# Kernel optimization log

Measured on AMD Instinct MI355X. Metric: run time of the kernel, lower is better.

The kernel has to match this reference:

```python
import jax, jax.numpy as jnp
import numpy as np

B, C, H, W = 128, 128, 32, 32
EPS = 1e-5


def _proj(x, w, b):
    # 1x1 conv: w [C_out, C_in], b [C_out]
    return jnp.einsum('oi,bihw->bohw', w, x) + b[None, :, None, None]


def _conv(x, w, pad):
    # x [B,Cin,H,W], w [Cout,Cin,k,k]
    return jax.lax.conv_general_dilated(
        x, w, window_strides=(1, 1), padding=[(pad, pad), (pad, pad)],
        dimension_numbers=('NCHW', 'OIHW', 'NCHW'))


def _ln(x, g, b):
    # LayerNorm over [C,H,W] per batch element
    mu = jnp.mean(x, axis=(1, 2, 3), keepdims=True)
    var = jnp.var(x, axis=(1, 2, 3), keepdims=True)
    return (x - mu) * jax.lax.rsqrt(var + EPS) * g[None] + b[None]


def _attn(q, k, v):
    # per (b,c) spatial matmul: [H,W]@[W,W] -> softmax -> @[W,W] -> softmax
    a = jax.nn.softmax(jnp.einsum('bchw,bcwk->bchk', q, k), axis=-1)
    return jax.nn.softmax(jnp.einsum('bchw,bcwk->bchk', a, v), axis=-1)


def setup_inputs() -> dict:
    key = jax.random.key(0)
    ks = iter(jax.random.split(key, 32))
    d = {}
    d['st'] = jax.random.normal(next(ks), (B, C, H, W), jnp.float32)
    d['phy'] = jax.random.normal(next(ks), (B, C, H, W), jnp.float32)
    s = 1.0 / np.sqrt(C)
    for nm in ['q_st', 'k_st', 'v_st', 'q_phy', 'k_phy', 'v_phy']:
        d['w' + nm] = jax.random.normal(next(ks), (C, C), jnp.float32) * s
        d['b' + nm] = jnp.zeros((C,), jnp.float32)
    for kk, nm in [(3, '3'), (5, '5'), (7, '7'), (1, '1')]:
        fan = 4 * C * kk * kk
        d['w' + nm] = jax.random.normal(next(ks), (C, 4 * C, kk, kk), jnp.float32) / np.sqrt(fan)
        d['g' + nm] = jnp.ones((C, H, W), jnp.float32)
        d['be' + nm] = jnp.zeros((C, H, W), jnp.float32)
    d['b1'] = jnp.zeros((C,), jnp.float32)
    return d


def reference(st, phy,
              wq_st, bq_st, wk_st, bk_st, wv_st, bv_st,
              wq_phy, bq_phy, wk_phy, bk_phy, wv_phy, bv_phy,
              w3, g3, be3, w5, g5, be5, w7, g7, be7,
              w1, b1, g1, be1):
    q_phy = _proj(phy, wq_phy, bq_phy)
    k_phy = _proj(phy, wk_phy, bk_phy)
    v_phy = _proj(phy, wv_phy, bv_phy)
    out_phy = _attn(q_phy, k_phy, v_phy) + phy

    q_st = _proj(st, wq_st, bq_st)
    k_st = _proj(st, wk_st, bk_st)
    v_st = _proj(st, wv_st, bv_st)
    out_st = _attn(q_st, k_st, v_st) + st

    out_st_phy = _attn(q_phy, k_st, v_st)
    out_phy_st = _attn(q_st, k_phy, v_phy)

    concat = jnp.concatenate([out_st, out_phy, out_st_phy, out_phy_st], axis=1)

    x1 = _ln(_conv(concat, w3, 1), g3, be3)
    x2 = _ln(_conv(concat, w5, 2), g5, be5)
    x3 = _ln(_conv(concat, w7, 3), g7, be7)
    out_mti = jax.nn.sigmoid((x1 + x2 + x3) / 3.0)
    out_att = _ln(_conv(concat, w1, 0) + b1[None, :, None, None], g1, be1)
    return out_mti + out_att
```

## Files before the change

### kernel.cpp

```cpp
#include <hip/hip_runtime.h>
#include <hip/hip_bf16.h>

typedef __hip_bfloat16 bf16;
typedef unsigned char u8;
typedef unsigned long long u64;
typedef __attribute__((ext_vector_type(8))) short short8;
typedef __attribute__((ext_vector_type(8))) int i32x8;
typedef __attribute__((ext_vector_type(16))) float f32x16;
#define DI __device__ __forceinline__

union BF8 { int4 v; short8 s; bf16 h[8]; };
union BF4 { u64 u; bf16 h[4]; };
union U32B { int4 v[2]; i32x8 w; };


DI u8 f32_fp8(float v) {
  return (u8)(__builtin_amdgcn_cvt_pk_fp8_f32(v, 0.f, 0, false) & 0xff);
}

__global__ __launch_bounds__(256) void prep_w_kernel(
    const float* __restrict__ w3, const float* __restrict__ w5,
    const float* __restrict__ w7, const float* __restrict__ w1,
    const float* __restrict__ wq_st, const float* __restrict__ wk_st,
    const float* __restrict__ wv_st, const float* __restrict__ wq_phy,
    const float* __restrict__ wk_phy, const float* __restrict__ wv_phy,
    u8* __restrict__ wf3, u8* __restrict__ wf5,
    u8* __restrict__ wf7, bf16* __restrict__ wb1, bf16* __restrict__ wp)
{
  const int N3 = 9 * 65536, N5 = 25 * 65536, N7 = 49 * 65536, N1 = 65536;
  const int NP = 6 * 16384;
  const int total = N3 + N5 + N7 + N1 + NP;
  for (int i = blockIdx.x * 256 + threadIdx.x; i < total; i += gridDim.x * 256) {
    if (i < N3 + N5 + N7) {
      const float* w; int k; int taps;
      u8* dst;
      if (i < N3)           { w = w3; k = i;            taps = 9;  dst = wf3; }
      else if (i < N3 + N5) { w = w5; k = i - N3;       taps = 25; dst = wf5; }
      else                  { w = w7; k = i - N3 - N5;  taps = 49; dst = wf7; }
      int tap = k >> 16, rem = k & 65535;
      int cc2 = rem >> 13, r2 = rem & 8191;
      int g = r2 >> 12, r3 = r2 & 4095;
      int oc = r3 >> 5, o = r3 & 31;
      int ic = (cc2 * 2 + g) * 32 + ((o >> 3) & 1) * 16 + ((o >> 4) & 1) * 8 + (o & 7);
      dst[k] = f32_fp8(w[(size_t)(oc * 512 + ic) * taps + tap] * 256.0f);
    } else if (i < N3 + N5 + N7 + N1) {
      int k = i - N3 - N5 - N7;
      int icg = k >> 10, oc = (k >> 3) & 127, j = k & 7;
      wb1[k] = __float2bfloat16(w1[(size_t)oc * 512 + icg * 8 + j]);
    } else {
      int k = i - N3 - N5 - N7 - N1;
      int m = k >> 14, r = k & 16383;
      float v;
      switch (m) {
        case 0: v = wq_st[r]; break;
        case 1: v = wk_st[r]; break;
        case 2: v = wv_st[r]; break;
        case 3: v = wq_phy[r]; break;
        case 4: v = wk_phy[r]; break;
        default: v = wv_phy[r]; break;
      }
      wp[k] = __float2bfloat16(v);
    }
  }
}

__global__ __launch_bounds__(256) void xpose_in_kernel(
    const float* __restrict__ st, const float* __restrict__ phy,
    bf16* __restrict__ Xt)
{
  __shared__ __align__(16) short Tb[64 * 72];
  const int x = blockIdx.x, b = blockIdx.y;
  const int t = x >> 5, rem = x & 31;
  const int ict = rem >> 4, post = rem & 15;
  const int ic0 = ict * 64, pos0 = post * 64;
  const int tid = threadIdx.x;
  const int rowi = tid >> 2, sub = tid & 3;
  const float* X = t ? phy : st;

  const float* src = X + ((size_t)b * 128 + ic0 + rowi) * 1024 + pos0 + sub * 16;
  #pragma unroll
  for (int q = 0; q < 4; ++q) {
    float4 v = *(const float4*)(src + q * 4);
    BF4 pk;
    pk.h[0] = __float2bfloat16(v.x); pk.h[1] = __float2bfloat16(v.y);
    pk.h[2] = __float2bfloat16(v.z); pk.h[3] = __float2bfloat16(v.w);
    *(u64*)&Tb[rowi * 72 + sub * 16 + q * 4] = pk.u;
  }
  __syncthreads();
  short tmp[16];
  #pragma unroll
  for (int j = 0; j < 16; ++j) tmp[j] = Tb[(sub * 16 + j) * 72 + rowi];
  bf16* dst = Xt + (((size_t)t * 128 + b) * 1024 + pos0 + rowi) * 128 + ic0 + sub * 16;
  *(int4*)dst       = ((int4*)tmp)[0];
  *(int4*)(dst + 8) = ((int4*)tmp)[1];
}

__global__ __launch_bounds__(256) void proj_mfma(
    const bf16* __restrict__ Xt, const bf16* __restrict__ wproj,
    const float* __restrict__ b0, const float* __restrict__ b1,
    const float* __restrict__ b2, const float* __restrict__ b3,
    const float* __restrict__ b4, const float* __restrict__ b5,
    bf16* __restrict__ pc, int cb)
{
  const int pt = blockIdx.x, b = blockIdx.y;
  const int tid = threadIdx.x, wave = tid >> 6, lane = tid & 63;
  const int col = lane & 31, kg = lane >> 5;
  const int pos = pt * 128 + wave * 32 + col;

  f32x16 acc[6];
  #pragma unroll
  for (int m = 0; m < 6; ++m)
    #pragma unroll
    for (int e = 0; e < 16; ++e) acc[m][e] = 0.f;

  const bf16* xst = Xt + ((size_t)b * 1024 + pos) * 128 + kg * 8;
  const bf16* xph = xst + (size_t)128 * 1024 * 128;
  const bf16* wl = wproj + (size_t)(cb + col) * 128 + kg * 8;

  #pragma unroll
  for (int kst = 0; kst < 8; ++kst) {
    short8 bst = *(const short8*)&xst[kst * 16];
    short8 bph = *(const short8*)&xph[kst * 16];
    #pragma unroll
    for (int m = 0; m < 6; ++m) {
      BF8 a; a.v = *(const int4*)&wl[(size_t)m * 16384 + kst * 16];
      acc[m] = __builtin_amdgcn_mfma_f32_32x32x16_bf16(a.s, m < 3 ? bst : bph, acc[m], 0, 0, 0);
    }
  }
  const float* biases[6] = { b0, b1, b2, b3, b4, b5 };
  #pragma unroll
  for (int m = 0; m < 6; ++m) {
    #pragma unroll
    for (int r = 0; r < 16; ++r) {
      const int ocl = (r & 3) + 8 * (r >> 2) + 4 * kg;
      float v = acc[m][r] + biases[m][cb + ocl];
      pc[(((size_t)m * 128 + b) * 32 + ocl) * 1024 + pos] = __float2bfloat16(v);
    }
  }
}

DI void softmax_rows(float p[16])
{
  #pragma unroll
  for (int r = 0; r < 16; ++r) {
    float m = p[r];
    m = fmaxf(m, __shfl_xor(m, 1));
    m = fmaxf(m, __shfl_xor(m, 2));
    m = fmaxf(m, __shfl_xor(m, 4));
    m = fmaxf(m, __shfl_xor(m, 8));
    m = fmaxf(m, __shfl_xor(m, 16));
    float e = __expf(p[r] - m);
    float s = e;
    s += __shfl_xor(s, 1); s += __shfl_xor(s, 2); s += __shfl_xor(s, 4);
    s += __shfl_xor(s, 8); s += __shfl_xor(s, 16);
    p[r] = __fdividef(e, s);
  }
}

template<bool U8OUT>
DI void attn_one_mfma(const BF8& qa0, const BF8& qa1,
                      const bf16* __restrict__ KT, const bf16* __restrict__ VT,
                      bf16* __restrict__ P,
                      const float* __restrict__ resid, void* outp, int lane)
{
  const int col = lane & 31, kg = lane >> 5;
  f32x16 acc;
  #pragma unroll
  for (int e = 0; e < 16; ++e) acc[e] = 0.f;
  BF8 kb0, kb1;
  kb0.v = *(const int4*)&KT[col * 40 + kg * 8];
  kb1.v = *(const int4*)&KT[col * 40 + 16 + kg * 8];
  acc = __builtin_amdgcn_mfma_f32_32x32x16_bf16(qa0.s, kb0.s, acc, 0, 0, 0);
  acc = __builtin_amdgcn_mfma_f32_32x32x16_bf16(qa1.s, kb1.s, acc, 0, 0, 0);
  float p[16];
  #pragma unroll
  for (int r = 0; r < 16; ++r) p[r] = acc[r];
  softmax_rows(p);
  __syncthreads();
  #pragma unroll
  for (int r = 0; r < 16; ++r) {
    int row = (r & 3) + 8 * (r >> 2) + 4 * kg;
    P[row * 40 + col] = __float2bfloat16(p[r]);
  }
  __syncthreads();
  BF8 pa0, pa1, vb0, vb1;
  pa0.v = *(const int4*)&P[col * 40 + kg * 8];
  pa1.v = *(const int4*)&P[col * 40 + 16 + kg * 8];
  vb0.v = *(const int4*)&VT[col * 40 + kg * 8];
  vb1.v = *(const int4*)&VT[col * 40 + 16 + kg * 8];
  #pragma unroll
  for (int e = 0; e < 16; ++e) acc[e] = 0.f;
  acc = __builtin_amdgcn_mfma_f32_32x32x16_bf16(pa0.s, vb0.s, acc, 0, 0, 0);
  acc = __builtin_amdgcn_mfma_f32_32x32x16_bf16(pa1.s, vb1.s, acc, 0, 0, 0);
  #pragma unroll
  for (int r = 0; r < 16; ++r) p[r] = acc[r];
  softmax_rows(p);
  if constexpr (!U8OUT) {
    bf16* op = (bf16*)outp;
    #pragma unroll
    for (int r = 0; r < 16; ++r) {
      int row = (r & 3) + 8 * (r >> 2) + 4 * kg;
      int off = row * 32 + col;
      op[off] = __float2bfloat16(p[r] + resid[off]);
    }
  } else {
    u8* op = (u8*)outp;
    #pragma unroll
    for (int r = 0; r < 16; ++r) {
      int row = (r & 3) + 8 * (r >> 2) + 4 * kg;
      op[row * 32 + col] = (u8)fminf(p[r] * 256.f + 0.5f, 255.f);
    }
  }
}

__global__ __launch_bounds__(64) void attn_mfma_kernel(
    const bf16* __restrict__ pc,
    const float* __restrict__ st, const float* __restrict__ phy,
    bf16* __restrict__ cA, u8* __restrict__ cB, int cb)
{
  __shared__ __align__(16) bf16 KTst[32 * 40], VTst[32 * 40];
  __shared__ __align__(16) bf16 KTph[32 * 40], VTph[32 * 40];
  __shared__ __align__(16) bf16 P[32 * 40];
  const int cl = blockIdx.x, b = blockIdx.y;
  const int c = cb + cl;
  const int lane = threadIdx.x;
  const size_t mstride = (size_t)128 * 32 * 1024;
  const bf16* p0 = pc + ((size_t)b * 32 + cl) * 1024;
  const size_t bc = ((size_t)b * 128 + c) * 1024;

  {
    const int w = lane >> 1, k0 = (lane & 1) * 16;
    const int off = w * 32 + k0;
    bf16* dsts[4] = { KTst, VTst, KTph, VTph };
    const int ms[4] = { 1, 2, 4, 5 };
    #pragma unroll
    for (int t = 0; t < 4; ++t) {
      BF8 r0, r1;
      r0.v = *(const int4*)&p0[(size_t)ms[t] * mstride + off];
      r1.v = *(const int4*)&p0[(size_t)ms[t] * mstride + off + 8];
      #pragma unroll
      for (int j = 0; j < 8; ++j) {
        dsts[t][(k0 + j) * 40 + w]     = r0.h[j];
        dsts[t][(k0 + 8 + j) * 40 + w] = r1.h[j];
      }
    }
  }
  const int col = lane & 31, kg = lane >> 5;
  BF8 qst0, qst1, qph0, qph1;
  qst0.v = *(const int4*)&p0[col * 32 + kg * 8];
  qst1.v = *(const int4*)&p0[col * 32 + 16 + kg * 8];
  qph0.v = *(const int4*)&p0[3 * mstride + col * 32 + kg * 8];
  qph1.v = *(const int4*)&p0[3 * mstride + col * 32 + 16 + kg * 8];
  __syncthreads();

  bf16* aA = cA + (size_t)b * 256 * 1024 + (size_t)c * 1024;
  u8*   aB = cB + (size_t)b * 256 * 1024 + (size_t)c * 1024;
  attn_one_mfma<false>(qst0, qst1, KTst, VTst, P, st + bc,  aA,          lane);
  attn_one_mfma<false>(qph0, qph1, KTph, VTph, P, phy + bc, aA + 131072, lane);
  attn_one_mfma<true >(qph0, qph1, KTst, VTst, P, nullptr,  aB,          lane);
  attn_one_mfma<true >(qst0, qst1, KTph, VTph, P, nullptr,  aB + 131072, lane);
}

__global__ __launch_bounds__(256) void transpose_kernel(
    const bf16* __restrict__ cA, const u8* __restrict__ cB,
    bf16* __restrict__ cAT, u8* __restrict__ cBT)
{
  __shared__ __align__(16) short Tb[64 * 72];
  __shared__ __align__(16) u8 T8[64 * 80];
  const int x = blockIdx.x, b = blockIdx.y;
  const int cht = x >> 4, post = x & 15;
  const int pos0 = post * 64;
  const int tid = threadIdx.x;
  const int rowi = tid >> 2, sub = tid & 3;

  if (cht < 4) {
    const int ch0 = cht * 64;
    const bf16* src = cA + ((size_t)b * 256 + ch0 + rowi) * 1024 + pos0 + sub * 16;
    *(int4*)&Tb[rowi * 72 + sub * 16]     = *(const int4*)src;
    *(int4*)&Tb[rowi * 72 + sub * 16 + 8] = *(const int4*)(src + 8);
    __syncthreads();
    short tmp[16];
    #pragma unroll
    for (int j = 0; j < 16; ++j) tmp[j] = Tb[(sub * 16 + j) * 72 + rowi];
    bf16* dst = cAT + ((size_t)b * 1024 + pos0 + rowi) * 256 + ch0 + sub * 16;
    *(int4*)dst       = ((int4*)tmp)[0];
    *(int4*)(dst + 8) = ((int4*)tmp)[1];
  } else {
    const int ch0 = (cht - 4) * 64;
    const u8* src = cB + ((size_t)b * 256 + ch0 + rowi) * 1024 + pos0 + sub * 16;
    *(int4*)&T8[rowi * 80 + sub * 16] = *(const int4*)src;
    __syncthreads();
    u8 tmp[16];
    #pragma unroll
    for (int j = 0; j < 16; ++j) tmp[j] = T8[(sub * 16 + j) * 80 + rowi];
    u8* dst = cBT + ((size_t)b * 1024 + pos0 + rowi) * 256 + ch0 + sub * 16;
    *(int4*)dst = *(int4*)tmp;
  }
}

__global__ __launch_bounds__(256) void to_fp8_kernel(
    const bf16* __restrict__ cAT, const u8* __restrict__ cBT,
    u8* __restrict__ cAT8)
{
  const int idx = blockIdx.x * 256 + threadIdx.x;
  const int g = idx & 31;
  const size_t bp = (size_t)(idx >> 5);
  const int c0 = g * 16;
  float v[16];
  if (c0 < 256) {
    BF8 lo, hi;
    lo.v = *(const int4*)&cAT[bp * 256 + c0];
    hi.v = *(const int4*)&cAT[bp * 256 + c0 + 8];
    #pragma unroll
    for (int j = 0; j < 8; ++j) {
      v[j]     = __bfloat162float(lo.h[j]) * 16.0f;
      v[8 + j] = __bfloat162float(hi.h[j]) * 16.0f;
    }
  } else {
    u64 raw0 = *(const u64*)&cBT[bp * 256 + (c0 - 256)];
    u64 raw1 = *(const u64*)&cBT[bp * 256 + (c0 - 256) + 8];
    #pragma unroll
    for (int j = 0; j < 8; ++j) {
      v[j]     = (float)((raw0 >> (8 * j)) & 255u) * 0.0625f;
      v[8 + j] = (float)((raw1 >> (8 * j)) & 255u) * 0.0625f;
    }
  }
  unsigned lo0 = (__builtin_amdgcn_cvt_pk_fp8_f32(v[0], v[1], 0, false) & 0xffff)
               | ((__builtin_amdgcn_cvt_pk_fp8_f32(v[2], v[3], 0, false) & 0xffff) << 16);
  unsigned hi0 = (__builtin_amdgcn_cvt_pk_fp8_f32(v[4], v[5], 0, false) & 0xffff)
               | ((__builtin_amdgcn_cvt_pk_fp8_f32(v[6], v[7], 0, false) & 0xffff) << 16);
  unsigned lo1 = (__builtin_amdgcn_cvt_pk_fp8_f32(v[8], v[9], 0, false) & 0xffff)
               | ((__builtin_amdgcn_cvt_pk_fp8_f32(v[10], v[11], 0, false) & 0xffff) << 16);
  unsigned hi1 = (__builtin_amdgcn_cvt_pk_fp8_f32(v[12], v[13], 0, false) & 0xffff)
               | ((__builtin_amdgcn_cvt_pk_fp8_f32(v[14], v[15], 0, false) & 0xffff) << 16);
  u64 run0 = (u64)lo0 | ((u64)hi0 << 32);
  u64 run1 = (u64)lo1 | ((u64)hi1 << 32);
  const int sp = (c0 >> 4) & 1;
  u8* d = cAT8 + bp * 512 + (c0 & ~31);
  *(u64*)(d + 8 * sp)      = run0;
  *(u64*)(d + 16 + 8 * sp) = run1;
}

template<int PCX, int NIT, int H0>
DI void stage_tile(const bf16* cAT, const u8* cBT, short* Xs,
                   int b, int r0, int ic0, int tid)
{
  for (int e = tid; e < NIT; e += 256) {
    int i = e / (PCX * 4);
    int rem = e - i * (PCX * 4);
    int cx = rem >> 2, part = rem & 3;
    int ir = r0 - H0 + i, c = cx - H0;
    int4 val = make_int4(0, 0, 0, 0);
    if ((unsigned)ir < 32u && (unsigned)c < 32u) {
      size_t pbase = ((size_t)b * 1024 + ir * 32 + c) * 256;
      if (ic0 < 256) {
        val = *(const int4*)&cAT[pbase + ic0 + part * 8];
      } else {
        u64 u = *(const u64*)&cBT[pbase + (ic0 - 256) + part * 8];
        BF8 t;
        #pragma unroll
        for (int j = 0; j < 8; ++j)
          t.h[j] = __float2bfloat16((float)((u >> (8 * j)) & 255u) * 0.00390625f);
        val = t.v;
      }
    }
    *(int4*)&Xs[(i * PCX + cx) * 40 + part * 8] = val;
  }
}

template<int KS>
__global__ __launch_bounds__(256, 2) void conv_mfma(
    const bf16* __restrict__ cAT, const u8* __restrict__ cBT,
    const bf16* __restrict__ wt, const float* __restrict__ bias,
    bf16* __restrict__ xout, float* __restrict__ partials)
{
  constexpr int H0 = KS / 2;
  constexpr int PCX = 32 + 2 * H0;
  constexpr int ROWS = 16 + 2 * H0;
  constexpr int NIT = ROWS * PCX * 4;
  __shared__ __align__(16) short Xs[ROWS * PCX * 40];
  __shared__ float rs[256], rq[256];
  const int h = blockIdx.x;
  const int logical = (h & 7) * 64 + (h >> 3);
  const int b = logical >> 2, tix = logical & 3;
  const int ot = tix >> 1, rt = tix & 1;
  const int oc0 = ot * 64, r0 = rt * 16;
  const int tid = threadIdx.x;
  const int wv = tid >> 6, lane = tid & 63;
  const int col = lane & 31, kg = lane >> 5;

  f32x16 acc[2][4];
  #pragma unroll
  for (int i = 0; i < 2; ++i)
    #pragma unroll
    for (int j = 0; j < 4; ++j)
      #pragma unroll
      for (int e = 0; e < 16; ++e) acc[i][j][e] = 0.f;

  for (int cc = 0; cc < 16; ++cc) {
    const int ic0 = cc * 32;
    stage_tile<PCX, NIT, H0>(cAT, cBT, Xs, b, r0, ic0, tid);
    __syncthreads();

    #pragma unroll 1
    for (int ky = 0; ky < KS; ++ky) {
      #pragma unroll
      for (int kx = 0; kx < KS; ++kx) {
        const int tap = ky * KS + kx;
        BF8 a[2][2];
        #pragma unroll
        for (int ob = 0; ob < 2; ++ob)
          #pragma unroll
          for (int kt = 0; kt < 2; ++kt) {
            int icg = cc * 4 + kt * 2 + kg;
            a[ob][kt].v = *(const int4*)&wt[(((size_t)tap * 64 + icg) * 128 + oc0 + ob * 32 + col) * 8];
          }
        #pragma unroll
        for (int rr = 0; rr < 4; ++rr) {
          int entry = ((wv * 4 + rr + ky) * PCX + col + kx) * 40;
          #pragma unroll
          for (int kt = 0; kt < 2; ++kt) {
            short8 bf = *(const short8*)&Xs[entry + (kt * 2 + kg) * 8];
            acc[0][rr] = __builtin_amdgcn_mfma_f32_32x32x16_bf16(a[0][kt].s, bf, acc[0][rr], 0, 0, 0);
            acc[1][rr] = __builtin_amdgcn_mfma_f32_32x32x16_bf16(a[1][kt].s, bf, acc[1][rr], 0, 0, 0);
          }
        }
      }
    }
    __syncthreads();
  }

  float lsum = 0.f, lsq = 0.f;
  #pragma unroll
  for (int ob = 0; ob < 2; ++ob)
    #pragma unroll
    for (int rr = 0; rr < 4; ++rr) {
      const int row = r0 + wv * 4 + rr;
      #pragma unroll
      for (int r = 0; r < 16; ++r) {
        const int oc = oc0 + ob * 32 + (r & 3) + 8 * (r >> 2) + 4 * kg;
        float v = acc[ob][rr][r];
        if (bias) v += bias[oc];
        xout[((size_t)b * 128 + oc) * 1024 + row * 32 + col] = __float2bfloat16(v);
        lsum += v; lsq += v * v;
      }
    }
  rs[tid] = lsum; rq[tid] = lsq;
  __syncthreads();
  for (int s = 128; s > 0; s >>= 1) {
    if (tid < s) { rs[tid] += rs[tid + s]; rq[tid] += rq[tid + s]; }
    __syncthreads();
  }
  if (tid == 0) {
    partials[((size_t)b * 4 + tix) * 2]     = rs[0];
    partials[((size_t)b * 4 + tix) * 2 + 1] = rq[0];
  }
}

template<int KS>
__global__ __launch_bounds__(256, 2) void conv_mx(
    const u8* __restrict__ cAT8, const u8* __restrict__ wf,
    bf16* __restrict__ xout, float* __restrict__ partials)
{
  constexpr int H0 = KS / 2;
  constexpr int PCX = 32 + 2 * H0;
  constexpr int ROWS = 16 + 2 * H0;
  constexpr int NIT = ROWS * PCX * 4;
  __shared__ __align__(16) u8 Xs[ROWS * PCX * 80];
  __shared__ float rs[256], rq[256];
  const int h = blockIdx.x;
  const int logical = (h & 7) * 64 + (h >> 3);
  const int b = logical >> 2, tix = logical & 3;
  const int ot = tix >> 1, rt = tix & 1;
  const int oc0 = ot * 64, r0 = rt * 16;
  const int tid = threadIdx.x;
  const int wv = tid >> 6, lane = tid & 63;
  const int col = lane & 31, g = lane >> 5;

  f32x16 acc[2][4];
  #pragma unroll
  for (int i = 0; i < 2; ++i)
    #pragma unroll
    for (int j = 0; j < 4; ++j)
      #pragma unroll
      for (int e = 0; e < 16; ++e) acc[i][j][e] = 0.f;

  for (int cc2 = 0; cc2 < 8; ++cc2) {
    for (int e = tid; e < NIT; e += 256) {
      int entry = e >> 2, hf = e & 3;
      int i = entry / PCX, cx = entry - i * PCX;
      int ir = r0 - H0 + i, c = cx - H0;
      int4 val = make_int4(0, 0, 0, 0);
      if ((unsigned)ir < 32u && (unsigned)c < 32u)
        val = *(const int4*)&cAT8[((size_t)b * 1024 + ir * 32 + c) * 512 + cc2 * 64 + hf * 16];
      *(int4*)&Xs[entry * 80 + hf * 16] = val;
    }
    __syncthreads();

    #pragma unroll 1
    for (int ky = 0; ky < KS; ++ky) {
      #pragma unroll
      for (int kx = 0; kx < KS; ++kx) {
        const int tap = ky * KS + kx;
        const size_t wbase = (((size_t)tap * 8 + cc2) * 2 + g) * 128;
        U32B a0, a1;
        a0.v[0] = *(const int4*)&wf[(wbase + oc0 + col) * 32];
        a0.v[1] = *(const int4*)&wf[(wbase + oc0 + col) * 32 + 16];
        a1.v[0] = *(const int4*)&wf[(wbase + oc0 + 32 + col) * 32];
        a1.v[1] = *(const int4*)&wf[(wbase + oc0 + 32 + col) * 32 + 16];
        #pragma unroll
        for (int rr = 0; rr < 4; ++rr) {
          const int ebase = ((wv * 4 + rr + ky) * PCX + col + kx) * 80 + g * 32;
          U32B bf;
          bf.v[0] = *(const int4*)&Xs[ebase];
          bf.v[1] = *(const int4*)&Xs[ebase + 16];
          acc[0][rr] = __builtin_amdgcn_mfma_scale_f32_32x32x64_f8f6f4(
              a0.w, bf.w, acc[0][rr], 0, 0, 0, 0x7f7f7f7f, 0, 0x7f7f7f7f);
          acc[1][rr] = __builtin_amdgcn_mfma_scale_f32_32x32x64_f8f6f4(
              a1.w, bf.w, acc[1][rr], 0, 0, 0, 0x7f7f7f7f, 0, 0x7f7f7f7f);
        }
      }
    }
    __syncthreads();
  }

  float lsum = 0.f, lsq = 0.f;
  #pragma unroll
  for (int ob = 0; ob < 2; ++ob)
    #pragma unroll
    for (int rr = 0; rr < 4; ++rr) {
      const int row = r0 + wv * 4 + rr;
      #pragma unroll
      for (int r = 0; r < 16; ++r) {
        const int oc = oc0 + ob * 32 + (r & 3) + 8 * (r >> 2) + 4 * g;
        float v = acc[ob][rr][r] * (1.0f / 4096.0f);
        xout[((size_t)b * 128 + oc) * 1024 + row * 32 + col] = __float2bfloat16(v);
        lsum += v; lsq += v * v;
      }
    }
  rs[tid] = lsum; rq[tid] = lsq;
  __syncthreads();
  for (int s = 128; s > 0; s >>= 1) {
    if (tid < s) { rs[tid] += rs[tid + s]; rq[tid] += rq[tid + s]; }
    __syncthreads();
  }
  if (tid == 0) {
    partials[((size_t)b * 4 + tix) * 2]     = rs[0];
    partials[((size_t)b * 4 + tix) * 2 + 1] = rq[0];
  }
}

__global__ __launch_bounds__(256) void final_kernel(
    const bf16* __restrict__ x3, const bf16* __restrict__ x5,
    const bf16* __restrict__ x7, const bf16* __restrict__ x1c,
    const float* __restrict__ p3, const float* __restrict__ p5,
    const float* __restrict__ p7, const float* __restrict__ p1,
    const float* __restrict__ g3, const float* __restrict__ be3,
    const float* __restrict__ g5, const float* __restrict__ be5,
    const float* __restrict__ g7, const float* __restrict__ be7,
    const float* __restrict__ g1, const float* __restrict__ be1,
    float* __restrict__ out)
{
  const int blk = blockIdx.x, b = blockIdx.y, tid = threadIdx.x;
  float s3 = 0, q3 = 0, s5 = 0, q5 = 0, s7 = 0, q7 = 0, s1 = 0, q1 = 0;
  #pragma unroll
  for (int i = 0; i < 4; ++i) {
    int o = (b * 4 + i) * 2;
    s3 += p3[o]; q3 += p3[o + 1];
    s5 += p5[o]; q5 += p5[o + 1];
    s7 += p7[o]; q7 += p7[o + 1];
    s1 += p1[o]; q1 += p1[o + 1];
  }
  const float inv = 1.0f / 131072.0f;
  float mu3 = s3 * inv, r3 = rsqrtf(fmaxf(q3 * inv - mu3 * mu3, 0.f) + 1e-5f);
  float mu5 = s5 * inv, r5 = rsqrtf(fmaxf(q5 * inv - mu5 * mu5, 0.f) + 1e-5f);
  float mu7 = s7 * inv, r7 = rsqrtf(fmaxf(q7 * inv - mu7 * mu7, 0.f) + 1e-5f);
  float mu1 = s1 * inv, r1 = rsqrtf(fmaxf(q1 * inv - mu1 * mu1, 0.f) + 1e-5f);
  const size_t bb = (size_t)b * 131072;
  for (int it = 0; it < 8; ++it) {
    int e0 = (it * 2048 + blk * 256 + tid) * 8;
    BF8 a3, a5, a7, a1;
    a3.v = *(const int4*)&x3[bb + e0];
    a5.v = *(const int4*)&x5[bb + e0];
    a7.v = *(const int4*)&x7[bb + e0];
    a1.v = *(const int4*)&x1c[bb + e0];
    float G3[8], B3[8], G5[8], B5[8], G7[8], B7[8], G1[8], B1[8];
    *(float4*)&G3[0] = *(const float4*)&g3[e0];  *(float4*)&G3[4] = *(const float4*)&g3[e0 + 4];
    *(float4*)&B3[0] = *(const float4*)&be3[e0]; *(float4*)&B3[4] = *(const float4*)&be3[e0 + 4];
    *(float4*)&G5[0] = *(const float4*)&g5[e0];  *(float4*)&G5[4] = *(const float4*)&g5[e0 + 4];
    *(float4*)&B5[0] = *(const float4*)&be5[e0]; *(float4*)&B5[4] = *(const float4*)&be5[e0 + 4];
    *(float4*)&G7[0] = *(const float4*)&g7[e0];  *(float4*)&G7[4] = *(const float4*)&g7[e0 + 4];
    *(float4*)&B7[0] = *(const float4*)&be7[e0]; *(float4*)&B7[4] = *(const float4*)&be7[e0 + 4];
    *(float4*)&G1[0] = *(const float4*)&g1[e0];  *(float4*)&G1[4] = *(const float4*)&g1[e0 + 4];
    *(float4*)&B1[0] = *(const float4*)&be1[e0]; *(float4*)&B1[4] = *(const float4*)&be1[e0 + 4];
    float res[8];
    #pragma unroll
    for (int j = 0; j < 8; ++j) {
      float v3 = (__bfloat162float(a3.h[j]) - mu3) * r3 * G3[j] + B3[j];
      float v5 = (__bfloat162float(a5.h[j]) - mu5) * r5 * G5[j] + B5[j];
      float v7 = (__bfloat162float(a7.h[j]) - mu7) * r7 * G7[j] + B7[j];
      float m = (v3 + v5 + v7) * (1.0f / 3.0f);
      float sg = 1.0f / (1.0f + __expf(-m));
      float v1 = (__bfloat162float(a1.h[j]) - mu1) * r1 * G1[j] + B1[j];
      res[j] = sg + v1;
    }
    *(float4*)&out[bb + e0]     = make_float4(res[0], res[1], res[2], res[3]);
    *(float4*)&out[bb + e0 + 4] = make_float4(res[4], res[5], res[6], res[7]);
  }
}

extern "C" void kernel_launch(void* const* d_in, const int* in_sizes, int n_in,
                              void* d_out, int out_size, void* d_ws, size_t ws_size,
                              hipStream_t stream)
{
  (void)in_sizes; (void)n_in; (void)out_size; (void)ws_size;
  const float* st     = (const float*)d_in[0];
  const float* phy    = (const float*)d_in[1];
  const float* wq_st  = (const float*)d_in[2];
  const float* bq_st  = (const float*)d_in[3];
  const float* wk_st  = (const float*)d_in[4];
  const float* bk_st  = (const float*)d_in[5];
  const float* wv_st  = (const float*)d_in[6];
  const float* bv_st  = (const float*)d_in[7];
  const float* wq_phy = (const float*)d_in[8];
  const float* bq_phy = (const float*)d_in[9];
  const float* wk_phy = (const float*)d_in[10];
  const float* bk_phy = (const float*)d_in[11];
  const float* wv_phy = (const float*)d_in[12];
  const float* bv_phy = (const float*)d_in[13];
  const float* w3  = (const float*)d_in[14];
  const float* g3  = (const float*)d_in[15];
  const float* be3 = (const float*)d_in[16];
  const float* w5  = (const float*)d_in[17];
  const float* g5  = (const float*)d_in[18];
  const float* be5 = (const float*)d_in[19];
  const float* w7  = (const float*)d_in[20];
  const float* g7  = (const float*)d_in[21];
  const float* be7 = (const float*)d_in[22];
  const float* w1  = (const float*)d_in[23];
  const float* g1  = (const float*)d_in[24];
  const float* be1 = (const float*)d_in[25];
  const float* b1  = (const float*)d_in[26];

  char* ws = (char*)d_ws;
  bf16* Xt        = (bf16*)ws;
  bf16* projchunk = (bf16*)(ws + 67108864ULL);
  bf16* cA        = (bf16*)(ws + 117440512ULL);
  u8*   cB        = (u8*)(ws + 184549376ULL);
  bf16* wproj     = (bf16*)(ws + 218103808ULL);
  bf16* cAT       = (bf16*)ws;
  u8*   cBT       = (u8*)(ws + 67108864ULL);
  u8*   cAT8      = (u8*)(ws + 117440512ULL);
  bf16* x1b       = (bf16*)(ws + 184549376ULL);
  bf16* x3b       = (bf16*)ws;
  bf16* x5b       = (bf16*)(ws + 33554432ULL);
  bf16* x7b       = (bf16*)(ws + 67108864ULL);
  float* parts    = (float*)(ws + 234881024ULL);
  u8*   wf3       = (u8*)(ws + 234913792ULL);
  u8*   wf5       = (u8*)(ws + 236093440ULL);
  u8*   wf7       = (u8*)(ws + 239370240ULL);
  bf16* wb1       = (bf16*)(ws + 245792768ULL);

  prep_w_kernel<<<dim3(2048), 256, 0, stream>>>(w3, w5, w7, w1,
      wq_st, wk_st, wv_st, wq_phy, wk_phy, wv_phy,
      wf3, wf5, wf7, wb1, wproj);
  xpose_in_kernel<<<dim3(64, 128), 256, 0, stream>>>(st, phy, Xt);

  for (int g = 0; g < 4; ++g) {
    proj_mfma<<<dim3(8, 128), 256, 0, stream>>>(Xt, wproj,
        bq_st, bk_st, bv_st, bq_phy, bk_phy, bv_phy, projchunk, g * 32);
    attn_mfma_kernel<<<dim3(32, 128), 64, 0, stream>>>(projchunk, st, phy,
        cA, cB, g * 32);
  }
  transpose_kernel<<<dim3(128, 128), 256, 0, stream>>>(cA, cB, cAT, cBT);
  to_fp8_kernel<<<dim3(16384), 256, 0, stream>>>(cAT, cBT, cAT8);

  conv_mfma<1><<<dim3(512), 256, 0, stream>>>(cAT, cBT, wb1, b1, x1b, parts + 6144);
  conv_mx<3><<<dim3(512), 256, 0, stream>>>(cAT8, wf3, x3b, parts);
  conv_mx<5><<<dim3(512), 256, 0, stream>>>(cAT8, wf5, x5b, parts + 2048);
  conv_mx<7><<<dim3(512), 256, 0, stream>>>(cAT8, wf7, x7b, parts + 4096);

  final_kernel<<<dim3(8, 128), 256, 0, stream>>>(x3b, x5b, x7b, x1b,
      parts, parts + 2048, parts + 4096, parts + 6144,
      g3, be3, g5, be5, g7, be7, g1, be1, (float*)d_out);
}
```

Baseline: 1.233 ms.

## Retile conv_mx blocks to all 128 output channels over 8 rows

Each block of the fp8 MFMA conv now covers all 128 output channels for an 8-row strip, where it used to cover 64 channels for a 16-row strip. Each wave loads its two input-row fragments from LDS once per tap and reuses them across four weight fragments. The smaller LDS halo tile allows three blocks per CU via the launch bounds. In exchange, each block reads the full weight set and the halo overhead per row grows, which raises redundant input staging, especially for KS=7.

```diff
diff --git a/kernel.cpp b/kernel.cpp
--- a/kernel.cpp
+++ b/kernel.cpp
@@ -458,30 +458,29 @@
 }
 
 template<int KS>
-__global__ __launch_bounds__(256, 2) void conv_mx(
+__global__ __launch_bounds__(256, 3) void conv_mx(
     const u8* __restrict__ cAT8, const u8* __restrict__ wf,
     bf16* __restrict__ xout, float* __restrict__ partials)
 {
   constexpr int H0 = KS / 2;
   constexpr int PCX = 32 + 2 * H0;
-  constexpr int ROWS = 16 + 2 * H0;
+  constexpr int ROWS = 8 + 2 * H0;
   constexpr int NIT = ROWS * PCX * 4;
   __shared__ __align__(16) u8 Xs[ROWS * PCX * 80];
   __shared__ float rs[256], rq[256];
   const int h = blockIdx.x;
   const int logical = (h & 7) * 64 + (h >> 3);
-  const int b = logical >> 2, tix = logical & 3;
-  const int ot = tix >> 1, rt = tix & 1;
-  const int oc0 = ot * 64, r0 = rt * 16;
+  const int b = logical >> 2, rt = logical & 3;
+  const int r0 = rt * 8;
   const int tid = threadIdx.x;
   const int wv = tid >> 6, lane = tid & 63;
   const int col = lane & 31, g = lane >> 5;
 
-  f32x16 acc[2][4];
-  #pragma unroll
-  for (int i = 0; i < 2; ++i)
-    #pragma unroll
-    for (int j = 0; j < 4; ++j)
+  f32x16 acc[4][2];
+  #pragma unroll
+  for (int i = 0; i < 4; ++i)
+    #pragma unroll
+    for (int j = 0; j < 2; ++j)
       #pragma unroll
       for (int e = 0; e < 16; ++e) acc[i][j][e] = 0.f;
 
@@ -503,21 +502,24 @@
       for (int kx = 0; kx < KS; ++kx) {
         const int tap = ky * KS + kx;
         const size_t wbase = (((size_t)tap * 8 + cc2) * 2 + g) * 128;
-        U32B a0, a1;
-        a0.v[0] = *(const int4*)&wf[(wbase + oc0 + col) * 32];
-        a0.v[1] = *(const int4*)&wf[(wbase + oc0 + col) * 32 + 16];
-        a1.v[0] = *(const int4*)&wf[(wbase + oc0 + 32 + col) * 32];
-        a1.v[1] = *(const int4*)&wf[(wbase + oc0 + 32 + col) * 32 + 16];
+        U32B bf0, bf1;
+        {
+          const int e0 = ((wv * 2 + 0 + ky) * PCX + col + kx) * 80 + g * 32;
+          const int e1 = ((wv * 2 + 1 + ky) * PCX + col + kx) * 80 + g * 32;
+          bf0.v[0] = *(const int4*)&Xs[e0];
+          bf0.v[1] = *(const int4*)&Xs[e0 + 16];
+          bf1.v[0] = *(const int4*)&Xs[e1];
+          bf1.v[1] = *(const int4*)&Xs[e1 + 16];
+        }
         #pragma unroll
-        for (int rr = 0; rr < 4; ++rr) {
-          const int ebase = ((wv * 4 + rr + ky) * PCX + col + kx) * 80 + g * 32;
-          U32B bf;
-          bf.v[0] = *(const int4*)&Xs[ebase];
-          bf.v[1] = *(const int4*)&Xs[ebase + 16];
-          acc[0][rr] = __builtin_amdgcn_mfma_scale_f32_32x32x64_f8f6f4(
-              a0.w, bf.w, acc[0][rr], 0, 0, 0, 0x7f7f7f7f, 0, 0x7f7f7f7f);
-          acc[1][rr] = __builtin_amdgcn_mfma_scale_f32_32x32x64_f8f6f4(
-              a1.w, bf.w, acc[1][rr], 0, 0, 0, 0x7f7f7f7f, 0, 0x7f7f7f7f);
+        for (int ob = 0; ob < 4; ++ob) {
+          U32B a;
+          a.v[0] = *(const int4*)&wf[(wbase + ob * 32 + col) * 32];
+          a.v[1] = *(const int4*)&wf[(wbase + ob * 32 + col) * 32 + 16];
+          acc[ob][0] = __builtin_amdgcn_mfma_scale_f32_32x32x64_f8f6f4(
+              a.w, bf0.w, acc[ob][0], 0, 0, 0, 0x7f7f7f7f, 0, 0x7f7f7f7f);
+          acc[ob][1] = __builtin_amdgcn_mfma_scale_f32_32x32x64_f8f6f4(
+              a.w, bf1.w, acc[ob][1], 0, 0, 0, 0x7f7f7f7f, 0, 0x7f7f7f7f);
         }
       }
     }
@@ -526,13 +528,13 @@
 
   float lsum = 0.f, lsq = 0.f;
   #pragma unroll
-  for (int ob = 0; ob < 2; ++ob)
-    #pragma unroll
-    for (int rr = 0; rr < 4; ++rr) {
-      const int row = r0 + wv * 4 + rr;
+  for (int ob = 0; ob < 4; ++ob)
+    #pragma unroll
+    for (int rr = 0; rr < 2; ++rr) {
+      const int row = r0 + wv * 2 + rr;
       #pragma unroll
       for (int r = 0; r < 16; ++r) {
-        const int oc = oc0 + ob * 32 + (r & 3) + 8 * (r >> 2) + 4 * g;
+        const int oc = ob * 32 + (r & 3) + 8 * (r >> 2) + 4 * g;
         float v = acc[ob][rr][r] * (1.0f / 4096.0f);
         xout[((size_t)b * 128 + oc) * 1024 + row * 32 + col] = __float2bfloat16(v);
         lsum += v; lsq += v * v;
@@ -545,8 +547,8 @@
     __syncthreads();
   }
   if (tid == 0) {
-    partials[((size_t)b * 4 + tix) * 2]     = rs[0];
-    partials[((size_t)b * 4 + tix) * 2 + 1] = rq[0];
+    partials[((size_t)b * 4 + rt) * 2]     = rs[0];
+    partials[((size_t)b * 4 + rt) * 2 + 1] = rq[0];
   }
 }
 
```

Measured after the change: 2.308 ms. 87.1% more time.
